# Kernel optimization log

Measured on AMD Instinct MI355X. Metric: run time of the kernel, lower is better.

The kernel has to match this reference:

```python
import jax, jax.numpy as jnp
import numpy as np

DIM = 256
HEADS = 8
HD = DIM // HEADS        # head_dim = 32
WS = 8                   # window_size (Wh = Ww = 8)
NEXP = 8                 # num_experts
HID = 128                # attr_hidden_size (router hidden)
SCALE = HD ** -0.5


def _window_partition(x, ws):
    # (B, H, W, C) -> (B * H//ws * W//ws, ws, ws, C)
    B, H, W, C = x.shape
    x = x.reshape(B, H // ws, ws, W // ws, ws, C)
    return x.transpose(0, 1, 3, 2, 4, 5).reshape(-1, ws, ws, C)


def _window_reverse(w, ws, B, H, W):
    # inverse of _window_partition
    C = w.shape[-1]
    x = w.reshape(B, H // ws, W // ws, ws, ws, C)
    return x.transpose(0, 1, 3, 2, 4, 5).reshape(B, H, W, C)


def _rope2(x):
    # 2D rotary embedding over a window: x (B*, Wh, Ww, d).
    # First d/2 channels rotated by row position, last d/2 by column position.
    B, Wh, Ww, d = x.shape
    d2 = d // 2

    def angles(L, dd):
        inv = 1.0 / (10000.0 ** (jnp.arange(0, dd, 2, dtype=jnp.float32) / dd))
        return jnp.arange(L, dtype=jnp.float32)[:, None] * inv[None, :]  # (L, dd//2)

    def rotate(v, ang, bshape):
        # v: (B, Wh, Ww, dd) pairs interleaved; ang broadcast as bshape
        p = v.reshape(*v.shape[:-1], -1, 2)
        c = jnp.cos(ang).reshape(bshape)
        s = jnp.sin(ang).reshape(bshape)
        o0 = p[..., 0] * c - p[..., 1] * s
        o1 = p[..., 0] * s + p[..., 1] * c
        return jnp.stack([o0, o1], axis=-1).reshape(v.shape)

    ah = angles(Wh, d2)  # (Wh, d2//2)
    aw = angles(Ww, d2)  # (Ww, d2//2)
    xh = rotate(x[..., :d2], ah, (1, Wh, 1, d2 // 2))
    xw = rotate(x[..., d2:], aw, (1, 1, Ww, d2 // 2))
    return jnp.concatenate([xh, xw], axis=-1)


def _moe_linear(xf, routes, w, b):
    # Top-1 dispatch: per-expert dense GEMM, masked select (jit-safe, static shapes).
    # xf: (T, in), routes: (T,) int, w: (E, out, in), b: (E, out)
    out = jnp.zeros((xf.shape[0], w.shape[1]), xf.dtype)
    for i in range(w.shape[0]):
        y = xf @ w[i].T + b[i]
        out = jnp.where((routes == i)[:, None], y, out)
    return out


def setup_inputs() -> dict:
    key = jax.random.key(0)
    ks = jax.random.split(key, 8)
    sc = 0.02
    return {
        "x": jax.random.normal(ks[0], (8, 64, 64, DIM), jnp.float32),
        "router_w1": jax.random.normal(ks[1], (HID, DIM), jnp.float32) * sc,
        "router_b1": jnp.zeros((HID,), jnp.float32),
        "router_w2": jax.random.normal(ks[2], (NEXP, HID), jnp.float32) * sc,
        "router_b2": jnp.zeros((NEXP,), jnp.float32),
        "qkv_w": jax.random.normal(ks[3], (NEXP, 3 * DIM, DIM), jnp.float32) * sc,
        "qkv_b": jnp.zeros((NEXP, 3 * DIM), jnp.float32),
        "proj_w": jax.random.normal(ks[4], (NEXP, DIM, DIM), jnp.float32) * sc,
        "proj_b": jnp.zeros((NEXP, DIM), jnp.float32),
    }


def reference(x, router_w1, router_b1, router_w2, router_b2,
              qkv_w, qkv_b, proj_w, proj_b):
    Bs, H, W, C = x.shape
    xf = x.reshape(-1, C)  # (T, C), T = Bs*H*W

    # --- Top-1 router (eval mode: no noise, no token dropping) ---
    h = jax.nn.relu(xf @ router_w1.T + router_b1)
    router_logits = h @ router_w2.T + router_b2          # (T, E)
    router_probs = jax.nn.softmax(router_logits, axis=-1)
    route_prob_max = jnp.max(router_probs, axis=-1)       # (T,)
    routes = jnp.argmax(router_probs, axis=-1)            # (T,)

    # --- per-expert QKV projection (grouped dispatch) ---
    qkv = _moe_linear(xf, routes, qkv_w, qkv_b)           # (T, 3C)
    qkv = qkv.reshape(Bs, H, W, 3 * C)

    # --- window partition (shift=0, dilated=1 -> no roll, mask=None) ---
    qw = _window_partition(qkv, WS).reshape(-1, WS * WS, 3 * C)
    B_, N, _ = qw.shape
    qkv5 = qw.reshape(B_, N, 3, HEADS, HD).transpose(2, 0, 3, 1, 4)  # (3,B_,h,N,hd)
    q, k, v = qkv5[0], qkv5[1], qkv5[2]

    # --- RoPE on q, k over the 2D window ---
    q = _rope2(q.reshape(-1, WS, WS, HD)).reshape(B_, HEADS, N, HD)
    k = _rope2(k.reshape(-1, WS, WS, HD)).reshape(B_, HEADS, N, HD)

    # --- windowed attention (moe_mask is all zeros in eval: no drops) ---
    attn = jax.nn.softmax((q * SCALE) @ k.swapaxes(-2, -1), axis=-1)  # (B_,h,N,N)
    out = (attn @ v).swapaxes(1, 2).reshape(B_, N, C)

    # --- window reverse ---
    out = _window_reverse(out.reshape(-1, WS, WS, C), WS, Bs, H, W)

    # --- per-expert output projection + Switch-style prob scaling ---
    of = _moe_linear(out.reshape(-1, C), routes, proj_w, proj_b)
    of = of * route_prob_max[:, None]
    return of.reshape(Bs, H, W, C)
```

## Files before the change

### kernel.cpp

```cpp
#include <hip/hip_runtime.h>
#include <hip/hip_bf16.h>

typedef unsigned short u16;
typedef unsigned int u32;
typedef __attribute__((ext_vector_type(8))) short short8;
typedef __attribute__((ext_vector_type(4))) float f32x4;

#define T_TOK 32768
#define SCALE_ATT 0.17677669529663687f

__device__ __forceinline__ u16 f2bf(float f){
  u32 u = __float_as_uint(f);
  u32 r = u + 0x7fffu + ((u >> 16) & 1u);
  return (u16)(r >> 16);
}
__device__ __forceinline__ float bf2f(u16 h){
  return __uint_as_float(((u32)h) << 16);
}

__device__ __forceinline__ int xcd_swz(int flat, int nwg){
  return (flat & 7) * (nwg >> 3) + (flat >> 3);
}

__device__ __forceinline__ void gl16(const u16* g, u16* l){
  __builtin_amdgcn_global_load_lds(
      (const __attribute__((address_space(1))) u32*)g,
      (__attribute__((address_space(3))) u32*)l, 16, 0, 0);
}

__global__ __launch_bounds__(256) void k_router(
    const float* __restrict__ x, const float* __restrict__ rw1,
    const float* __restrict__ b1, const float* __restrict__ w2, const float* __restrict__ b2,
    int* __restrict__ routes, float* __restrict__ pmax, int* __restrict__ counts,
    u16* __restrict__ x_bf,
    const float* __restrict__ qkvw, u16* __restrict__ qw_bf,
    const float* __restrict__ projw, u16* __restrict__ pw_bf)
{
  __shared__ __align__(16) char smem[64*132*4];
  int tid = threadIdx.x;

  if (blockIdx.x >= 512){
    int b = blockIdx.x - 512;
    if (b < 1536){
      int i = b * 256 + tid;
      float4 v = ((const float4*)qkvw)[i];
      ushort4 o;
      o.x = f2bf(v.x); o.y = f2bf(v.y); o.z = f2bf(v.z); o.w = f2bf(v.w);
      ((ushort4*)qw_bf)[i] = o;
    } else {
      int i = (b - 1536) * 256 + tid;
      float4 v = ((const float4*)projw)[i];
      ushort4 o;
      o.x = f2bf(v.x); o.y = f2bf(v.y); o.z = f2bf(v.z); o.w = f2bf(v.w);
      ((ushort4*)pw_bf)[i] = o;
    }
    return;
  }

  u16* Ah = (u16*)smem;
  u16* Al = Ah + 2560;
  u16* Bh = Al + 2560;
  u16* Bl = Bh + 5120;
  float* Hs = (float*)smem;
  __shared__ int lhist[8];

  int t0 = blockIdx.x * 64;
  int wv = tid >> 6, lane = tid & 63, quad = lane >> 4, l16 = lane & 15;
  if (tid < 8) lhist[tid] = 0;

  int arow = tid >> 2, acg = tid & 3;
  int brow = tid >> 1, bhalf = tid & 1;

  f32x4 acc[4][2];
  #pragma unroll
  for (int i = 0; i < 4; ++i)
    #pragma unroll
    for (int j = 0; j < 2; ++j)
      #pragma unroll
      for (int rr = 0; rr < 4; ++rr) acc[i][j][rr] = 0.f;

  const float* gx_base = x + (size_t)(t0 + arow) * 256 + acg * 8;
  u16* gxb_base = x_bf + (size_t)(t0 + arow) * 256 + acg * 8;
  const float* gw_base = rw1 + (size_t)brow * 256 + bhalf * 16;

  float4 v0 = *(const float4*)gx_base;
  float4 v1 = *(const float4*)(gx_base + 4);
  float4 wf0 = *(const float4*)(gw_base     );
  float4 wf1 = *(const float4*)(gw_base +  4);
  float4 wf2 = *(const float4*)(gw_base +  8);
  float4 wf3 = *(const float4*)(gw_base + 12);

  for (int kt = 0; kt < 8; ++kt){
    ushort4 h0, h1, l0, l1;
    h0.x = f2bf(v0.x); h0.y = f2bf(v0.y); h0.z = f2bf(v0.z); h0.w = f2bf(v0.w);
    h1.x = f2bf(v1.x); h1.y = f2bf(v1.y); h1.z = f2bf(v1.z); h1.w = f2bf(v1.w);
    l0.x = f2bf(v0.x - bf2f(h0.x)); l0.y = f2bf(v0.y - bf2f(h0.y));
    l0.z = f2bf(v0.z - bf2f(h0.z)); l0.w = f2bf(v0.w - bf2f(h0.w));
    l1.x = f2bf(v1.x - bf2f(h1.x)); l1.y = f2bf(v1.y - bf2f(h1.y));
    l1.z = f2bf(v1.z - bf2f(h1.z)); l1.w = f2bf(v1.w - bf2f(h1.w));
    *(ushort4*)(gxb_base + kt*32)     = h0;
    *(ushort4*)(gxb_base + kt*32 + 4) = h1;
    ushort4 wh[4], wl[4];
    {
      float4 wf;
      wf = wf0;
      wh[0].x = f2bf(wf.x); wh[0].y = f2bf(wf.y); wh[0].z = f2bf(wf.z); wh[0].w = f2bf(wf.w);
      wl[0].x = f2bf(wf.x - bf2f(wh[0].x)); wl[0].y = f2bf(wf.y - bf2f(wh[0].y));
      wl[0].z = f2bf(wf.z - bf2f(wh[0].z)); wl[0].w = f2bf(wf.w - bf2f(wh[0].w));
      wf = wf1;
      wh[1].x = f2bf(wf.x); wh[1].y = f2bf(wf.y); wh[1].z = f2bf(wf.z); wh[1].w = f2bf(wf.w);
      wl[1].x = f2bf(wf.x - bf2f(wh[1].x)); wl[1].y = f2bf(wf.y - bf2f(wh[1].y));
      wl[1].z = f2bf(wf.z - bf2f(wh[1].z)); wl[1].w = f2bf(wf.w - bf2f(wh[1].w));
      wf = wf2;
      wh[2].x = f2bf(wf.x); wh[2].y = f2bf(wf.y); wh[2].z = f2bf(wf.z); wh[2].w = f2bf(wf.w);
      wl[2].x = f2bf(wf.x - bf2f(wh[2].x)); wl[2].y = f2bf(wf.y - bf2f(wh[2].y));
      wl[2].z = f2bf(wf.z - bf2f(wh[2].z)); wl[2].w = f2bf(wf.w - bf2f(wh[2].w));
      wf = wf3;
      wh[3].x = f2bf(wf.x); wh[3].y = f2bf(wf.y); wh[3].z = f2bf(wf.z); wh[3].w = f2bf(wf.w);
      wl[3].x = f2bf(wf.x - bf2f(wh[3].x)); wl[3].y = f2bf(wf.y - bf2f(wh[3].y));
      wl[3].z = f2bf(wf.z - bf2f(wh[3].z)); wl[3].w = f2bf(wf.w - bf2f(wh[3].w));
    }
    __syncthreads();
    *(ushort4*)&Ah[arow*40 + acg*8    ] = h0;
    *(ushort4*)&Ah[arow*40 + acg*8 + 4] = h1;
    *(ushort4*)&Al[arow*40 + acg*8    ] = l0;
    *(ushort4*)&Al[arow*40 + acg*8 + 4] = l1;
    #pragma unroll
    for (int q = 0; q < 4; ++q){
      *(ushort4*)&Bh[brow*40 + bhalf*16 + q*4] = wh[q];
      *(ushort4*)&Bl[brow*40 + bhalf*16 + q*4] = wl[q];
    }
    __syncthreads();
    if (kt < 7){
      v0  = *(const float4*)(gx_base + (kt+1)*32);
      v1  = *(const float4*)(gx_base + (kt+1)*32 + 4);
      wf0 = *(const float4*)(gw_base + (kt+1)*32);
      wf1 = *(const float4*)(gw_base + (kt+1)*32 + 4);
      wf2 = *(const float4*)(gw_base + (kt+1)*32 + 8);
      wf3 = *(const float4*)(gw_base + (kt+1)*32 + 12);
    }
    short8 ah[4], al[4], bhf[2], blf[2];
    #pragma unroll
    for (int i = 0; i < 4; ++i){
      ah[i] = *(const short8*)&Ah[(i*16 + l16)*40 + quad*8];
      al[i] = *(const short8*)&Al[(i*16 + l16)*40 + quad*8];
    }
    #pragma unroll
    for (int j = 0; j < 2; ++j){
      bhf[j] = *(const short8*)&Bh[(wv*32 + j*16 + l16)*40 + quad*8];
      blf[j] = *(const short8*)&Bl[(wv*32 + j*16 + l16)*40 + quad*8];
    }
    #pragma unroll
    for (int i = 0; i < 4; ++i)
      #pragma unroll
      for (int j = 0; j < 2; ++j){
        acc[i][j] = __builtin_amdgcn_mfma_f32_16x16x32_bf16(ah[i], bhf[j], acc[i][j], 0, 0, 0);
        acc[i][j] = __builtin_amdgcn_mfma_f32_16x16x32_bf16(ah[i], blf[j], acc[i][j], 0, 0, 0);
        acc[i][j] = __builtin_amdgcn_mfma_f32_16x16x32_bf16(al[i], bhf[j], acc[i][j], 0, 0, 0);
      }
  }
  __syncthreads();

  #pragma unroll
  for (int i = 0; i < 4; ++i)
    #pragma unroll
    for (int j = 0; j < 2; ++j){
      int col = wv*32 + j*16 + l16;
      float bb = b1[col];
      #pragma unroll
      for (int rr = 0; rr < 4; ++rr){
        float h = acc[i][j][rr] + bb;
        Hs[(i*16 + quad*4 + rr)*132 + col] = h > 0.f ? h : 0.f;
      }
    }
  __syncthreads();

  #pragma unroll
  for (int pass = 0; pass < 2; ++pass){
    int mtok = (tid >> 3) + pass * 32;
    int e = tid & 7;
    const float4* w2r = (const float4*)(w2 + e * 128);
    float l = b2[e];
    #pragma unroll
    for (int k4 = 0; k4 < 32; ++k4){
      float4 w = w2r[k4];
      int k = k4 * 4;
      l = fmaf(Hs[mtok*132+k  ], w.x, l);
      l = fmaf(Hs[mtok*132+k+1], w.y, l);
      l = fmaf(Hs[mtok*132+k+2], w.z, l);
      l = fmaf(Hs[mtok*132+k+3], w.w, l);
    }
    float mv = l; int mi = e;
    #pragma unroll
    for (int off = 1; off < 8; off <<= 1){
      float ov = __shfl_xor(mv, off, 64);
      int   oi = __shfl_xor(mi, off, 64);
      if (ov > mv || (ov == mv && oi < mi)){ mv = ov; mi = oi; }
    }
    float sum = expf(l - mv);
    #pragma unroll
    for (int off = 1; off < 8; off <<= 1) sum += __shfl_xor(sum, off, 64);
    if (e == 0){
      int t = t0 + mtok;
      routes[t] = mi;
      pmax[t] = 1.0f / sum;
      atomicAdd(&lhist[mi], 1);
    }
  }
  __syncthreads();
  if (tid < 8 && lhist[tid] > 0) atomicAdd(&counts[tid], lhist[tid]);
}

__global__ __launch_bounds__(256) void k_scatter(
    const int* __restrict__ routes, const int* __restrict__ counts,
    int* __restrict__ cursors, int* __restrict__ sorted, int* __restrict__ rank,
    int* __restrict__ offs)
{
  __shared__ int lc[8], lb[8], so[9];
  int tid = threadIdx.x;
  if (tid == 0){
    int o = 0; so[0] = 0;
    #pragma unroll
    for (int e = 0; e < 8; ++e){ o += ((counts[e] + 127) >> 7) << 7; so[e+1] = o; }
  }
  if (tid < 8) lc[tid] = 0;
  __syncthreads();
  int t = blockIdx.x * 256 + tid;
  int e = routes[t];
  int rl = atomicAdd(&lc[e], 1);
  __syncthreads();
  if (tid < 8 && lc[tid] > 0) lb[tid] = atomicAdd(&cursors[tid], lc[tid]);
  __syncthreads();
  int pos = so[e] + lb[e] + rl;
  sorted[pos] = t;
  rank[t] = pos;
  if (blockIdx.x == 0 && tid < 9) offs[tid] = so[tid];
}

template<int NOUT, bool PROJ, int NB, int NWG>
__global__ __launch_bounds__(256) void k_gemm(
    const u16* __restrict__ A, const u16* __restrict__ W,
    const float* __restrict__ bias, const int* __restrict__ sidx,
    const int* __restrict__ offs, const float* __restrict__ pmax,
    u16* __restrict__ outb, float* __restrict__ outf)
{
  __shared__ __align__(1024) u16 As[3][4096];
  __shared__ __align__(1024) u16 Bs[3][4096];
  int tid = threadIdx.x;
  int flat = blockIdx.y * NB + blockIdx.x;
  int logical = xcd_swz(flat, NWG);
  int m0 = (logical / NB) * 128;
  int n0 = (logical % NB) * 128;
  int total = offs[8];
  if (m0 >= total) return;
  int e = 0;
  #pragma unroll
  for (int i = 1; i < 8; ++i) if (m0 >= offs[i]) e = i;

  int wv = tid >> 6, lane = tid & 63, quad = lane >> 4, l16 = lane & 15;
  int wrow = (wv >> 1) * 64, wcol = (wv & 1) * 64;

  int srow = wv*16 + (lane >> 2);
  int cg = (lane & 3) ^ ((srow >> 1) & 3);
  const u16 *ag0, *ag1;
  if (PROJ){
    ag0 = A + (size_t)(m0 + srow) * 256 + cg * 8;
    ag1 = A + (size_t)(m0 + srow + 64) * 256 + cg * 8;
  } else {
    int tA0 = sidx[m0 + srow];      if (tA0 < 0) tA0 = 0;
    int tA1 = sidx[m0 + srow + 64]; if (tA1 < 0) tA1 = 0;
    ag0 = A + (size_t)tA0 * 256 + cg * 8;
    ag1 = A + (size_t)tA1 * 256 + cg * 8;
  }
  int pc = (srow >> 4) + (srow & 15) * 4;
  const u16* bg0 = W + ((size_t)e * NOUT + n0 + pc) * 256 + cg * 8;
  const u16* bg1 = W + ((size_t)e * NOUT + n0 + 64 + pc) * 256 + cg * 8;

  f32x4 acc[4][4];
  #pragma unroll
  for (int i = 0; i < 4; ++i)
    #pragma unroll
    for (int j = 0; j < 4; ++j)
      #pragma unroll
      for (int r = 0; r < 4; ++r) acc[i][j][r] = 0.f;

  int qsw8 = (quad ^ ((l16 >> 1) & 3)) * 8;

#define STAGE_KT(kt, buf) do { \
    u16* a_lo = (u16*)((char*)&As[(buf)][0] + wv*1024); \
    u16* b_lo = (u16*)((char*)&Bs[(buf)][0] + wv*1024); \
    gl16(ag0 + (kt)*32, a_lo); \
    gl16(ag1 + (kt)*32, (u16*)((char*)a_lo + 4096)); \
    gl16(bg0 + (kt)*32, b_lo); \
    gl16(bg1 + (kt)*32, (u16*)((char*)b_lo + 4096)); \
  } while(0)

  STAGE_KT(0, 0);
  STAGE_KT(1, 1);

  #pragma unroll
  for (int kt = 0; kt < 8; ++kt){
    const int cur = kt % 3;
    if (kt < 7) asm volatile("s_waitcnt vmcnt(4) lgkmcnt(0)" ::: "memory");
    else        asm volatile("s_waitcnt vmcnt(0) lgkmcnt(0)" ::: "memory");
    __builtin_amdgcn_sched_barrier(0);
    __builtin_amdgcn_s_barrier();
    __builtin_amdgcn_sched_barrier(0);
    if (kt < 6) STAGE_KT(kt+2, (kt+2)%3);
    short8 af[4], bfv[4];
    #pragma unroll
    for (int i = 0; i < 4; ++i)
      af[i] = *(const short8*)&As[cur][(wrow + i*16 + l16)*32 + qsw8];
    #pragma unroll
    for (int j = 0; j < 4; ++j)
      bfv[j] = *(const short8*)&Bs[cur][(wcol + j*16 + l16)*32 + qsw8];
    #pragma unroll
    for (int i = 0; i < 4; ++i)
      #pragma unroll
      for (int j = 0; j < 4; ++j)
        acc[i][j] = __builtin_amdgcn_mfma_f32_16x16x32_bf16(af[i], bfv[j], acc[i][j], 0, 0, 0);
  }
#undef STAGE_KT

  float4 bj4 = *(const float4*)&bias[e*NOUT + n0 + wcol + l16*4];
  if (PROJ){
    #pragma unroll
    for (int i = 0; i < 4; ++i){
      #pragma unroll
      for (int ri = 0; ri < 4; ++ri){
        int row = wrow + i*16 + quad*4 + ri;
        int t = sidx[m0 + row];
        if (t < 0) continue;
        float pm = pmax[t];
        float4 ov;
        ov.x = (acc[i][0][ri] + bj4.x) * pm;
        ov.y = (acc[i][1][ri] + bj4.y) * pm;
        ov.z = (acc[i][2][ri] + bj4.z) * pm;
        ov.w = (acc[i][3][ri] + bj4.w) * pm;
        *(float4*)&outf[(size_t)t * NOUT + n0 + wcol + l16*4] = ov;
      }
    }
  } else {
    int col0 = n0 + wcol + l16*4;
    bool isqk = (col0 < 512);
    float inv0 = 0.f, inv1 = 0.f;
    float qsc = (col0 < 256) ? SCALE_ATT : 1.0f;
    if (isqk){
      int p0 = (col0 & 15) >> 1;
      inv0 = __expf(-1.1512925465f * (float)p0);
      inv1 = inv0 * 0.31622776601683794f;
    }
    int sel  = col0 >> 8;
    int head = (col0 >> 5) & 7;
    int ch   = col0 & 31;
    size_t hb = ((size_t)(sel * 8 + head) * 512) * 2048 + ch;
    #pragma unroll
    for (int i = 0; i < 4; ++i){
      #pragma unroll
      for (int ri = 0; ri < 4; ++ri){
        int row = wrow + i*16 + quad*4 + ri;
        int t = sidx[m0 + row];
        if (t < 0) continue;
        float vx = acc[i][0][ri] + bj4.x;
        float vy = acc[i][1][ri] + bj4.y;
        float vz = acc[i][2][ri] + bj4.z;
        float vw = acc[i][3][ri] + bj4.w;
        if (isqk){
          float pos = (float)((col0 & 16) ? (t & 7) : ((t >> 6) & 7));
          float a0r = pos * inv0, a1r = pos * inv1;
          float s0, c0s, s1, c1s;
          __sincosf(a0r, &s0, &c0s);
          __sincosf(a1r, &s1, &c1s);
          float r0 = (vx*c0s - vy*s0) * qsc;
          float r1 = (vx*s0 + vy*c0s) * qsc;
          float r2 = (vz*c1s - vw*s1) * qsc;
          float r3 = (vz*s1 + vw*c1s) * qsc;
          vx = r0; vy = r1; vz = r2; vw = r3;
        }
        int win = (t >> 12) * 64 + ((t >> 9) & 7) * 8 + ((t >> 3) & 7);
        int n   = ((t >> 6) & 7) * 8 + (t & 7);
        uint2 ov;
        ov.x = (u32)f2bf(vx) | ((u32)f2bf(vy) << 16);
        ov.y = (u32)f2bf(vz) | ((u32)f2bf(vw) << 16);
        *(uint2*)&outb[hb + (size_t)win * 2048 + n * 32] = ov;
      }
    }
  }
}

__global__ __launch_bounds__(64, 3) void k_attn(const u16* __restrict__ qkv,
                                                const int* __restrict__ rank,
                                                u16* __restrict__ attn_s)
{
  __shared__ __align__(16) u16 Ps[64*72];
  __shared__ __align__(16) u16 Vt[32*72];

  int lane = threadIdx.x;
  int quad = lane >> 4, l16 = lane & 15;
  int wh = xcd_swz(blockIdx.x, 4096);
  int head = wh >> 9, win = wh & 511;
  int b = win >> 6, wy = (win >> 3) & 7, wx = win & 7;
  int tb = b*4096 + wy*512 + wx*8;

  const u16* qbase = qkv + (size_t)(head * 512 + win) * 2048;
  const u16* kbase = qbase + (size_t)8 * 512 * 2048;
  const u16* vbase = qbase + (size_t)16 * 512 * 2048;

  int rk[4][4];
  #pragma unroll
  for (int i = 0; i < 4; ++i)
    #pragma unroll
    for (int rr = 0; rr < 4; ++rr){
      int m = i*16 + quad*4 + rr;
      rk[i][rr] = rank[tb + (m >> 3) * 64 + (m & 7)];
    }

  short8 qf[4], kf[4];
  #pragma unroll
  for (int i = 0; i < 4; ++i){
    qf[i] = *(const short8*)(qbase + (i*16 + l16)*32 + quad*8);
    kf[i] = *(const short8*)(kbase + (i*16 + l16)*32 + quad*8);
  }
  uint4 va[4];
  #pragma unroll
  for (int h = 0; h < 4; ++h)
    va[h] = *(const uint4*)(vbase + h*512 + l16*32 + quad*8);

  f32x4 sa[4][4];
  #pragma unroll
  for (int i = 0; i < 4; ++i)
    #pragma unroll
    for (int j = 0; j < 4; ++j){
      #pragma unroll
      for (int rr = 0; rr < 4; ++rr) sa[i][j][rr] = 0.f;
      sa[i][j] = __builtin_amdgcn_mfma_f32_16x16x32_bf16(qf[i], kf[j], sa[i][j], 0, 0, 0);
    }

  f32x4 rs[4];
  #pragma unroll
  for (int i = 0; i < 4; ++i)
    #pragma unroll
    for (int rr = 0; rr < 4; ++rr){
      float e0 = __expf(sa[i][0][rr]);
      float e1 = __expf(sa[i][1][rr]);
      float e2 = __expf(sa[i][2][rr]);
      float e3 = __expf(sa[i][3][rr]);
      rs[i][rr] = (e0 + e1) + (e2 + e3);
      uint2 pk;
      pk.x = (u32)f2bf(e0) | ((u32)f2bf(e1) << 16);
      pk.y = (u32)f2bf(e2) | ((u32)f2bf(e3) << 16);
      *(uint2*)&Ps[(i*16 + quad*4 + rr)*72 + l16*4] = pk;
    }
  #pragma unroll
  for (int i = 0; i < 4; ++i)
    #pragma unroll
    for (int rr = 0; rr < 4; ++rr){
      #pragma unroll
      for (int off = 1; off < 16; off <<= 1)
        rs[i][rr] += __shfl_xor(rs[i][rr], off, 64);
    }

  u32* vu = (u32*)va;
  #pragma unroll
  for (int h = 0; h < 4; ++h){
    int pn = l16 * 4 + h;
    #pragma unroll
    for (int w = 0; w < 4; ++w){
      u32 vv = vu[h*4 + w];
      Vt[(quad*8 + 2*w    )*72 + pn] = (u16)(vv & 0xffff);
      Vt[(quad*8 + 2*w + 1)*72 + pn] = (u16)(vv >> 16);
    }
  }

  f32x4 oa[4][2];
  #pragma unroll
  for (int i = 0; i < 4; ++i)
    #pragma unroll
    for (int rr = 0; rr < 4; ++rr){ oa[i][0][rr] = 0.f; oa[i][1][rr] = 0.f; }
  #pragma unroll
  for (int ks = 0; ks < 2; ++ks){
    short8 vf0 = *(const short8*)&Vt[(     l16)*72 + ks*32 + quad*8];
    short8 vf1 = *(const short8*)&Vt[(16 + l16)*72 + ks*32 + quad*8];
    #pragma unroll
    for (int i = 0; i < 4; ++i){
      short8 pf = *(const short8*)&Ps[(i*16 + l16)*72 + ks*32 + quad*8];
      oa[i][0] = __builtin_amdgcn_mfma_f32_16x16x32_bf16(pf, vf0, oa[i][0], 0, 0, 0);
      oa[i][1] = __builtin_amdgcn_mfma_f32_16x16x32_bf16(pf, vf1, oa[i][1], 0, 0, 0);
    }
  }

  #pragma unroll
  for (int i = 0; i < 4; ++i)
    #pragma unroll
    for (int rr = 0; rr < 4; ++rr){
      float inv = __builtin_amdgcn_rcpf(rs[i][rr]);
      int pos = rk[i][rr];
      u16* op = attn_s + (size_t)pos * 256 + head * 32 + l16;
      op[0]  = f2bf(oa[i][0][rr] * inv);
      op[16] = f2bf(oa[i][1][rr] * inv);
    }
}

extern "C" void kernel_launch(void* const* d_in, const int* in_sizes, int n_in,
                              void* d_out, int out_size, void* d_ws, size_t ws_size,
                              hipStream_t stream){
  const float* x     = (const float*)d_in[0];
  const float* rw1   = (const float*)d_in[1];
  const float* rb1   = (const float*)d_in[2];
  const float* rw2   = (const float*)d_in[3];
  const float* rb2   = (const float*)d_in[4];
  const float* qkvw  = (const float*)d_in[5];
  const float* qkvb  = (const float*)d_in[6];
  const float* projw = (const float*)d_in[7];
  const float* projb = (const float*)d_in[8];
  float* out = (float*)d_out;

  char* ws = (char*)d_ws;
  u16*   x_bf    = (u16*)(ws);
  u16*   qkv_bf  = (u16*)(ws + 16777216);
  u16*   attn_s  = (u16*)(ws + 67108864);
  u16*   qw_bf   = (u16*)(ws + 84410368);
  u16*   pw_bf   = (u16*)(ws + 87556096);
  int*   routes  = (int*)(ws + 88604672);
  float* pmaxp   = (float*)(ws + 88735744);
  int*   sorted  = (int*)(ws + 88866816);
  int*   rank    = (int*)(ws + 89001984);
  int*   counts  = (int*)(ws + 89133056);
  int*   cursors = (int*)(ws + 89133056 + 32);
  int*   offs    = (int*)(ws + 89133056 + 64);

  hipMemsetAsync(counts, 0, 64, stream);
  hipMemsetAsync(sorted, 0xFF, 135168, stream);
  k_router<<<2560, 256, 0, stream>>>(x, rw1, rb1, rw2, rb2, routes, pmaxp, counts,
                                     x_bf, qkvw, qw_bf, projw, pw_bf);
  k_scatter<<<128, 256, 0, stream>>>(routes, counts, cursors, sorted, rank, offs);
  k_gemm<768, false, 6, 1584><<<dim3(6, 264), 256, 0, stream>>>(
      x_bf, qw_bf, qkvb, sorted, offs, nullptr, qkv_bf, nullptr);
  k_attn<<<4096, 64, 0, stream>>>(qkv_bf, rank, attn_s);
  k_gemm<256, true, 2, 528><<<dim3(2, 264), 256, 0, stream>>>(
      attn_s, pw_bf, projb, sorted, offs, pmaxp, nullptr, out);
}
```

Measured before the change: 196.4 us.

## Precompute router W1 bf16 split and replace global atomics with per-block histograms

Adds a small kernel that splits the router's first-layer weight into bf16 high and low parts once, so each router block loads them directly instead of recomputing the split every k-step. The router now writes per-block expert histograms instead of doing global atomics on counts. The scatter kernel computes totals and prefix offsets from those histograms, which removes the cursor atomics and both hipMemsetAsync calls; block 0 writes the -1 padding of sorted itself. This trades two memsets and atomic contention for one extra tiny launch and a redundant histogram scan in every scatter block.

Result: no change. 195.3 us, median of 2 (-0.6%).

```diff
diff --git a/kernel.cpp b/kernel.cpp
--- a/kernel.cpp
+++ b/kernel.cpp
@@ -28,10 +28,23 @@
       (__attribute__((address_space(3))) u32*)l, 16, 0, 0);
 }
 
+__global__ __launch_bounds__(256) void k_prep_w1(
+    const float* __restrict__ rw1, u16* __restrict__ w1h, u16* __restrict__ w1l)
+{
+  int i = blockIdx.x * 256 + threadIdx.x;
+  float4 v = ((const float4*)rw1)[i];
+  ushort4 h, l;
+  h.x = f2bf(v.x); h.y = f2bf(v.y); h.z = f2bf(v.z); h.w = f2bf(v.w);
+  l.x = f2bf(v.x - bf2f(h.x)); l.y = f2bf(v.y - bf2f(h.y));
+  l.z = f2bf(v.z - bf2f(h.z)); l.w = f2bf(v.w - bf2f(h.w));
+  ((ushort4*)w1h)[i] = h;
+  ((ushort4*)w1l)[i] = l;
+}
+
 __global__ __launch_bounds__(256) void k_router(
-    const float* __restrict__ x, const float* __restrict__ rw1,
+    const float* __restrict__ x, const u16* __restrict__ w1h, const u16* __restrict__ w1l,
     const float* __restrict__ b1, const float* __restrict__ w2, const float* __restrict__ b2,
-    int* __restrict__ routes, float* __restrict__ pmax, int* __restrict__ counts,
+    int* __restrict__ routes, float* __restrict__ pmax, int* __restrict__ hist,
     u16* __restrict__ x_bf,
     const float* __restrict__ qkvw, u16* __restrict__ qw_bf,
     const float* __restrict__ projw, u16* __restrict__ pw_bf)
@@ -81,14 +94,15 @@
 
   const float* gx_base = x + (size_t)(t0 + arow) * 256 + acg * 8;
   u16* gxb_base = x_bf + (size_t)(t0 + arow) * 256 + acg * 8;
-  const float* gw_base = rw1 + (size_t)brow * 256 + bhalf * 16;
+  const u16* gwh_base = w1h + (size_t)brow * 256 + bhalf * 16;
+  const u16* gwl_base = w1l + (size_t)brow * 256 + bhalf * 16;
 
   float4 v0 = *(const float4*)gx_base;
   float4 v1 = *(const float4*)(gx_base + 4);
-  float4 wf0 = *(const float4*)(gw_base     );
-  float4 wf1 = *(const float4*)(gw_base +  4);
-  float4 wf2 = *(const float4*)(gw_base +  8);
-  float4 wf3 = *(const float4*)(gw_base + 12);
+  uint4 wh0 = *(const uint4*)(gwh_base);
+  uint4 wh1 = *(const uint4*)(gwh_base + 8);
+  uint4 wl0 = *(const uint4*)(gwl_base);
+  uint4 wl1 = *(const uint4*)(gwl_base + 8);
 
   for (int kt = 0; kt < 8; ++kt){
     ushort4 h0, h1, l0, l1;
@@ -100,44 +114,23 @@
     l1.z = f2bf(v1.z - bf2f(h1.z)); l1.w = f2bf(v1.w - bf2f(h1.w));
     *(ushort4*)(gxb_base + kt*32)     = h0;
     *(ushort4*)(gxb_base + kt*32 + 4) = h1;
-    ushort4 wh[4], wl[4];
-    {
-      float4 wf;
-      wf = wf0;
-      wh[0].x = f2bf(wf.x); wh[0].y = f2bf(wf.y); wh[0].z = f2bf(wf.z); wh[0].w = f2bf(wf.w);
-      wl[0].x = f2bf(wf.x - bf2f(wh[0].x)); wl[0].y = f2bf(wf.y - bf2f(wh[0].y));
-      wl[0].z = f2bf(wf.z - bf2f(wh[0].z)); wl[0].w = f2bf(wf.w - bf2f(wh[0].w));
-      wf = wf1;
-      wh[1].x = f2bf(wf.x); wh[1].y = f2bf(wf.y); wh[1].z = f2bf(wf.z); wh[1].w = f2bf(wf.w);
-      wl[1].x = f2bf(wf.x - bf2f(wh[1].x)); wl[1].y = f2bf(wf.y - bf2f(wh[1].y));
-      wl[1].z = f2bf(wf.z - bf2f(wh[1].z)); wl[1].w = f2bf(wf.w - bf2f(wh[1].w));
-      wf = wf2;
-      wh[2].x = f2bf(wf.x); wh[2].y = f2bf(wf.y); wh[2].z = f2bf(wf.z); wh[2].w = f2bf(wf.w);
-      wl[2].x = f2bf(wf.x - bf2f(wh[2].x)); wl[2].y = f2bf(wf.y - bf2f(wh[2].y));
-      wl[2].z = f2bf(wf.z - bf2f(wh[2].z)); wl[2].w = f2bf(wf.w - bf2f(wh[2].w));
-      wf = wf3;
-      wh[3].x = f2bf(wf.x); wh[3].y = f2bf(wf.y); wh[3].z = f2bf(wf.z); wh[3].w = f2bf(wf.w);
-      wl[3].x = f2bf(wf.x - bf2f(wh[3].x)); wl[3].y = f2bf(wf.y - bf2f(wh[3].y));
-      wl[3].z = f2bf(wf.z - bf2f(wh[3].z)); wl[3].w = f2bf(wf.w - bf2f(wh[3].w));
-    }
     __syncthreads();
     *(ushort4*)&Ah[arow*40 + acg*8    ] = h0;
     *(ushort4*)&Ah[arow*40 + acg*8 + 4] = h1;
     *(ushort4*)&Al[arow*40 + acg*8    ] = l0;
     *(ushort4*)&Al[arow*40 + acg*8 + 4] = l1;
-    #pragma unroll
-    for (int q = 0; q < 4; ++q){
-      *(ushort4*)&Bh[brow*40 + bhalf*16 + q*4] = wh[q];
-      *(ushort4*)&Bl[brow*40 + bhalf*16 + q*4] = wl[q];
-    }
+    *(uint4*)&Bh[brow*40 + bhalf*16    ] = wh0;
+    *(uint4*)&Bh[brow*40 + bhalf*16 + 8] = wh1;
+    *(uint4*)&Bl[brow*40 + bhalf*16    ] = wl0;
+    *(uint4*)&Bl[brow*40 + bhalf*16 + 8] = wl1;
     __syncthreads();
     if (kt < 7){
       v0  = *(const float4*)(gx_base + (kt+1)*32);
       v1  = *(const float4*)(gx_base + (kt+1)*32 + 4);
-      wf0 = *(const float4*)(gw_base + (kt+1)*32);
-      wf1 = *(const float4*)(gw_base + (kt+1)*32 + 4);
-      wf2 = *(const float4*)(gw_base + (kt+1)*32 + 8);
-      wf3 = *(const float4*)(gw_base + (kt+1)*32 + 12);
+      wh0 = *(const uint4*)(gwh_base + (kt+1)*32);
+      wh1 = *(const uint4*)(gwh_base + (kt+1)*32 + 8);
+      wl0 = *(const uint4*)(gwl_base + (kt+1)*32);
+      wl1 = *(const uint4*)(gwl_base + (kt+1)*32 + 8);
     }
     short8 ah[4], al[4], bhf[2], blf[2];
     #pragma unroll
@@ -208,33 +201,45 @@
     }
   }
   __syncthreads();
-  if (tid < 8 && lhist[tid] > 0) atomicAdd(&counts[tid], lhist[tid]);
+  if (tid < 8) hist[blockIdx.x * 8 + tid] = lhist[tid];
 }
 
 __global__ __launch_bounds__(256) void k_scatter(
-    const int* __restrict__ routes, const int* __restrict__ counts,
-    int* __restrict__ cursors, int* __restrict__ sorted, int* __restrict__ rank,
-    int* __restrict__ offs)
+    const int* __restrict__ routes, const int* __restrict__ hist,
+    int* __restrict__ sorted, int* __restrict__ rank, int* __restrict__ offs)
 {
-  __shared__ int lc[8], lb[8], so[9];
-  int tid = threadIdx.x;
+  __shared__ int s_tot[8], s_pre[8], so[9], lc[8];
+  int tid = threadIdx.x, b = blockIdx.x;
+  if (tid < 8){ s_tot[tid] = 0; s_pre[tid] = 0; lc[tid] = 0; }
+  __syncthreads();
+  int e8 = tid & 7, r0 = tid >> 3;
+  int tot = 0, pre = 0;
+  for (int rb = r0; rb < 512; rb += 32){
+    int v = hist[rb * 8 + e8];
+    tot += v;
+    if (rb < b * 4) pre += v;
+  }
+  atomicAdd(&s_tot[e8], tot);
+  atomicAdd(&s_pre[e8], pre);
+  __syncthreads();
   if (tid == 0){
     int o = 0; so[0] = 0;
     #pragma unroll
-    for (int e = 0; e < 8; ++e){ o += ((counts[e] + 127) >> 7) << 7; so[e+1] = o; }
-  }
-  if (tid < 8) lc[tid] = 0;
+    for (int e = 0; e < 8; ++e){ o += ((s_tot[e] + 127) >> 7) << 7; so[e+1] = o; }
+  }
   __syncthreads();
-  int t = blockIdx.x * 256 + tid;
+  int t = b * 256 + tid;
   int e = routes[t];
   int rl = atomicAdd(&lc[e], 1);
-  __syncthreads();
-  if (tid < 8 && lc[tid] > 0) lb[tid] = atomicAdd(&cursors[tid], lc[tid]);
-  __syncthreads();
-  int pos = so[e] + lb[e] + rl;
+  int pos = so[e] + s_pre[e] + rl;
   sorted[pos] = t;
   rank[t] = pos;
-  if (blockIdx.x == 0 && tid < 9) offs[tid] = so[tid];
+  if (b == 0){
+    if (tid < 9) offs[tid] = so[tid];
+    #pragma unroll
+    for (int e2 = 0; e2 < 8; ++e2)
+      for (int i = so[e2] + s_tot[e2] + tid; i < so[e2+1]; i += 256) sorted[i] = -1;
+  }
 }
 
 template<int NOUT, bool PROJ, int NB, int NWG>
@@ -518,6 +523,8 @@
   char* ws = (char*)d_ws;
   u16*   x_bf    = (u16*)(ws);
   u16*   qkv_bf  = (u16*)(ws + 16777216);
+  u16*   w1h     = (u16*)(ws + 67108864);
+  u16*   w1l     = w1h + 32768;
   u16*   attn_s  = (u16*)(ws + 67108864);
   u16*   qw_bf   = (u16*)(ws + 84410368);
   u16*   pw_bf   = (u16*)(ws + 87556096);
@@ -525,15 +532,13 @@
   float* pmaxp   = (float*)(ws + 88735744);
   int*   sorted  = (int*)(ws + 88866816);
   int*   rank    = (int*)(ws + 89001984);
-  int*   counts  = (int*)(ws + 89133056);
-  int*   cursors = (int*)(ws + 89133056 + 32);
-  int*   offs    = (int*)(ws + 89133056 + 64);
-
-  hipMemsetAsync(counts, 0, 64, stream);
-  hipMemsetAsync(sorted, 0xFF, 135168, stream);
-  k_router<<<2560, 256, 0, stream>>>(x, rw1, rb1, rw2, rb2, routes, pmaxp, counts,
+  int*   hist    = (int*)(ws + 89133056);
+  int*   offs    = (int*)(ws + 89149440);
+
+  k_prep_w1<<<32, 256, 0, stream>>>(rw1, w1h, w1l);
+  k_router<<<2560, 256, 0, stream>>>(x, w1h, w1l, rb1, rw2, rb2, routes, pmaxp, hist,
                                      x_bf, qkvw, qw_bf, projw, pw_bf);
-  k_scatter<<<128, 256, 0, stream>>>(routes, counts, cursors, sorted, rank, offs);
+  k_scatter<<<128, 256, 0, stream>>>(routes, hist, sorted, rank, offs);
   k_gemm<768, false, 6, 1584><<<dim3(6, 264), 256, 0, stream>>>(
       x_bf, qw_bf, qkvb, sorted, offs, nullptr, qkv_bf, nullptr);
   k_attn<<<4096, 64, 0, stream>>>(qkv_bf, rank, attn_s);
```
